# Kernel tuning notes

Measured on AMD Instinct MI355X. Metric: run time of the kernel, lower is better.

The kernel has to match this reference:

```python
import jax, jax.numpy as jnp
import numpy as np

B, Q, V, H, U = 4, 256, 2048, 512, 128

def setup_inputs() -> dict:
    key = jax.random.key(0)
    ks = jax.random.split(key, 5)
    return {
        "queries": jax.random.normal(ks[0], (B, Q, H), dtype=jnp.float32),
        "values": jax.random.normal(ks[1], (B, V, H), dtype=jnp.float32),
        "w1": jax.random.normal(ks[2], (H, U), dtype=jnp.float32) / np.sqrt(H),
        "w2": jax.random.normal(ks[3], (H, U), dtype=jnp.float32) / np.sqrt(H),
        "v": jax.random.normal(ks[4], (U,), dtype=jnp.float32) / np.sqrt(U),
    }

def reference(queries, values, w1, w2, v):
    # Project queries and values first (cheap GEMMs), then broadcast-add.
    pq = jnp.einsum("bqh,hu->bqu", queries, w1)          # [B,Q,U]
    pv = jnp.einsum("bvh,hu->bvu", values, w2)           # [B,V,U]
    # added_qv: [B,Q,V,U] -- the large intermediate the original materializes
    scores = jnp.einsum("bqvu,u->bqv", jnp.tanh(pq[:, :, None, :] + pv[:, None, :, :]), v)
    attn = jax.nn.softmax(scores, axis=-1)               # softmax over V (last axis, as tf.nn.softmax)
    return jnp.einsum("bqv,bvh->bqh", attn, values)      # [B,Q,H]
```

## Files before the change

### kernel.cpp

```cpp
#include <hip/hip_runtime.h>

#define BB 4
#define QQ 256
#define VV 2048
#define HH 512
#define UU 128

#define C2E   2.8853900817779268f
#define LOG2E 1.4426950408889634f

__device__ __forceinline__ void fma4(float4& a, float s, const float4& w) {
    a.x = fmaf(s, w.x, a.x);
    a.y = fmaf(s, w.y, a.y);
    a.z = fmaf(s, w.z, a.z);
    a.w = fmaf(s, w.w, a.w);
}
__device__ __forceinline__ void fma2s(float2& a, float s, const float2& w) {
    a.x = fmaf(s, w.x, a.x);
    a.y = fmaf(s, w.y, a.y);
}
__device__ __forceinline__ float2 rcp2(float2 x) {
    return make_float2(__builtin_amdgcn_rcpf(x.x), __builtin_amdgcn_rcpf(x.y));
}
__device__ __forceinline__ float2 mul2(float2 a, float2 b) { return make_float2(a.x*b.x, a.y*b.y); }
__device__ __forceinline__ float2 muls(float2 a, float s)  { return make_float2(a.x*s, a.y*s); }
__device__ __forceinline__ float2 fma2(float2 a, float2 b, float2 c) {
    return make_float2(fmaf(a.x, b.x, c.x), fmaf(a.y, b.y, c.y));
}
__device__ __forceinline__ float2 fmas(float2 a, float s, float2 c) {
    return make_float2(fmaf(a.x, s, c.x), fmaf(a.y, s, c.y));
}

__global__ __launch_bounds__(128) void proj_kernel(const float* __restrict__ queries,
                                                   const float* __restrict__ values,
                                                   const float* __restrict__ w1,
                                                   const float* __restrict__ w2,
                                                   float* __restrict__ pqI,
                                                   float* __restrict__ pvI,
                                                   float* __restrict__ denom) {
    __shared__ float smem[32 * 20 + 32 * 128];
    float (*As)[20] = (float(*)[20])smem;
    float* Ws = smem + 32 * 20;
    float (*Ls)[20] = (float(*)[20])smem;

    const int bid = blockIdx.x;
    const int tid = threadIdx.x;
    if (bid == 0) {
        *(float4*)&denom[tid * 8]     = make_float4(0.f, 0.f, 0.f, 0.f);
        *(float4*)&denom[tid * 8 + 4] = make_float4(0.f, 0.f, 0.f, 0.f);
    }

    const bool isv = (bid < 512);
    const float* A; const float* W; int b, r0, ROWS; float* Ob;
    if (isv) {
        b = bid >> 7; r0 = (bid & 127) * 16;
        A = values + ((size_t)(b * VV + r0)) * HH;  W = w2;
        Ob = pvI + (size_t)b * UU * VV;  ROWS = VV;
    } else {
        const int q = bid - 512;
        b = q >> 4; r0 = (q & 15) * 16;
        A = queries + ((size_t)(b * QQ + r0)) * HH; W = w1;
        Ob = pqI + (size_t)b * UU * QQ;  ROWS = QQ;
    }

    const int tx = tid & 31;
    const int ty = tid >> 5;
    float4 acc[4];
#pragma unroll
    for (int j = 0; j < 4; j++) acc[j] = make_float4(0.f, 0.f, 0.f, 0.f);

    for (int k0 = 0; k0 < HH; k0 += 32) {
        {
            const int r = tid >> 3, kk4 = (tid & 7) * 4;
            const float4 a = *(const float4*)&A[(size_t)r * HH + k0 + kk4];
            As[kk4 + 0][r] = a.x; As[kk4 + 1][r] = a.y;
            As[kk4 + 2][r] = a.z; As[kk4 + 3][r] = a.w;
        }
#pragma unroll
        for (int t = 0; t < 8; t++) {
            const int f = tid + t * 128;
            const int kk = f >> 5, u4 = (f & 31) * 4;
            *(float4*)&Ws[kk * 128 + u4] = *(const float4*)&W[(size_t)(k0 + kk) * UU + u4];
        }
        __syncthreads();
#pragma unroll
        for (int kk = 0; kk < 32; kk++) {
            const float4 a = *(const float4*)&As[kk][ty * 4];
            const float4 w = *(const float4*)&Ws[kk * 128 + tx * 4];
            fma4(acc[0], a.x, w);
            fma4(acc[1], a.y, w);
            fma4(acc[2], a.z, w);
            fma4(acc[3], a.w, w);
        }
        __syncthreads();
    }
#pragma unroll
    for (int j = 0; j < 4; j++) {
        const float aa[4] = {acc[j].x, acc[j].y, acc[j].z, acc[j].w};
#pragma unroll
        for (int i = 0; i < 4; i++)
            Ls[tx * 4 + i][ty * 4 + j] = __builtin_amdgcn_exp2f(aa[i] * C2E);
    }
    __syncthreads();
#pragma unroll
    for (int t = 0; t < 4; t++) {
        const int idx = tid + t * 128;
        const int g = idx >> 4, r = idx & 15;
        float4 o;
        o.x = Ls[4 * g + 0][r]; o.y = Ls[4 * g + 1][r];
        o.z = Ls[4 * g + 2][r]; o.w = Ls[4 * g + 3][r];
        *(float4*)&Ob[((size_t)g * ROWS + r0 + r) * 4] = o;
    }
}

__global__ __launch_bounds__(256, 4) void fused_kernel(const float* __restrict__ pqI,
                                                       const float* __restrict__ pvI,
                                                       const float* __restrict__ vvec,
                                                       const float* __restrict__ values,
                                                       float* __restrict__ slab,
                                                       float* __restrict__ denom) {
    __shared__ float att[128][16];
    __shared__ float wred[2][16];
    const int tid = threadIdx.x;
    const int bid = blockIdx.x;
    const int vs = bid & 15, qb = (bid >> 4) & 15, b = bid >> 8;
    const int qbase = qb * 16, vbase = vs * 128;

    const int vloc = tid & 127, uh = tid >> 7;
    const int v = vbase + vloc;

    float vsum = 0.0f;
#pragma unroll
    for (int u4 = 0; u4 < UU; u4 += 4) {
        const float4 t = *(const float4*)&vvec[u4];
        vsum += t.x + t.y + t.z + t.w;
    }

    const float* pv4 = pvI + (size_t)b * UU * VV + (size_t)v * 4;
    const float* pq4 = pqI + (size_t)b * UU * QQ + (size_t)qbase * 4;

    float2 acc[8];
#pragma unroll
    for (int p = 0; p < 8; p++) acc[p] = make_float2(0.f, 0.f);

    const int G0 = uh * 16;
    float4 ev = *(const float4*)&pv4[(size_t)G0 * VV * 4];

    for (int g = 0; g < 16; g++) {
        const int G = G0 + g;
        const float* eqp = &pq4[(size_t)G * QQ * 4];
        float4 evn;
        if (g < 15) evn = *(const float4*)&pv4[(size_t)(G + 1) * VV * 4];
        const float4 wq = *(const float4*)&vvec[G * 4];
        const float w0 = 2.f * wq.x, w1 = 2.f * wq.y;
        const float w2 = 2.f * wq.z, w3 = 2.f * wq.w;
#pragma unroll
        for (int p = 0; p < 8; p++) {
            const float4 e0 = *(const float4*)&eqp[(2 * p) * 4];
            const float4 e1 = *(const float4*)&eqp[(2 * p + 1) * 4];
            const float2 a1 = make_float2(fmaf(e0.x, ev.x, 1.f), fmaf(e1.x, ev.x, 1.f));
            const float2 b1 = make_float2(fmaf(e0.y, ev.y, 1.f), fmaf(e1.y, ev.y, 1.f));
            const float2 c1 = make_float2(fmaf(e0.z, ev.z, 1.f), fmaf(e1.z, ev.z, 1.f));
            const float2 d1 = make_float2(fmaf(e0.w, ev.w, 1.f), fmaf(e1.w, ev.w, 1.f));
            const float2 pab = mul2(a1, b1), pcd = mul2(c1, d1);
            const float2 nab = fmas(a1, w1, muls(b1, w0));
            const float2 ncd = fmas(c1, w3, muls(d1, w2));
            const float2 num = fma2(nab, pcd, mul2(ncd, pab));
            const float2 den = mul2(pab, pcd);
            acc[p] = fma2(num, rcp2(den), acc[p]);
        }
        ev = evn;
    }

    if (uh == 1) {
#pragma unroll
        for (int p = 0; p < 8; p++)
            *(float2*)&att[vloc][2 * p] = acc[p];
    }
    __syncthreads();
    if (uh == 0) {
#pragma unroll
        for (int p = 0; p < 8; p++) {
            const float2 hi = *(const float2*)&att[vloc][2 * p];
            float2 e;
            e.x = __builtin_amdgcn_exp2f((vsum - (acc[p].x + hi.x)) * LOG2E);
            e.y = __builtin_amdgcn_exp2f((vsum - (acc[p].y + hi.y)) * LOG2E);
            *(float2*)&att[vloc][2 * p] = e;
            acc[p] = e;
        }
#pragma unroll
        for (int off = 1; off < 64; off <<= 1) {
#pragma unroll
            for (int p = 0; p < 8; p++) {
                acc[p].x += __shfl_xor(acc[p].x, off, 64);
                acc[p].y += __shfl_xor(acc[p].y, off, 64);
            }
        }
        if ((tid & 63) == 0) {
            const int w = tid >> 6;
#pragma unroll
            for (int p = 0; p < 8; p++) {
                wred[w][2 * p + 0] = acc[p].x;
                wred[w][2 * p + 1] = acc[p].y;
            }
        }
    }
    __syncthreads();
    if (tid < 16)
        atomicAdd(&denom[b * QQ + qbase + tid], wred[0][tid] + wred[1][tid]);

    const int h0 = tid * 2;
    const float* vp = values + ((size_t)(b * VV + vbase)) * HH + h0;

    float2 oacc[16];
#pragma unroll
    for (int j = 0; j < 16; j++) oacc[j] = make_float2(0.f, 0.f);

#pragma unroll 2
    for (int vv = 0; vv < 128; vv++) {
        const float2 w = *(const float2*)&vp[(size_t)vv * HH];
        const float4 a0 = *(const float4*)&att[vv][0];
        const float4 a1 = *(const float4*)&att[vv][4];
        const float4 a2 = *(const float4*)&att[vv][8];
        const float4 a3 = *(const float4*)&att[vv][12];
        fma2s(oacc[0],  a0.x, w); fma2s(oacc[1],  a0.y, w);
        fma2s(oacc[2],  a0.z, w); fma2s(oacc[3],  a0.w, w);
        fma2s(oacc[4],  a1.x, w); fma2s(oacc[5],  a1.y, w);
        fma2s(oacc[6],  a1.z, w); fma2s(oacc[7],  a1.w, w);
        fma2s(oacc[8],  a2.x, w); fma2s(oacc[9],  a2.y, w);
        fma2s(oacc[10], a2.z, w); fma2s(oacc[11], a2.w, w);
        fma2s(oacc[12], a3.x, w); fma2s(oacc[13], a3.y, w);
        fma2s(oacc[14], a3.z, w); fma2s(oacc[15], a3.w, w);
    }

    float* sp = slab + (size_t)vs * (BB * QQ * HH);
#pragma unroll
    for (int j = 0; j < 16; j++) {
        *(float2*)&sp[((size_t)(b * QQ + qbase + j)) * HH + h0] = oacc[j];
    }
}

__global__ __launch_bounds__(256) void reduce_kernel(const float* __restrict__ slab,
                                                     const float* __restrict__ denom,
                                                     float* __restrict__ out) {
    const int i = blockIdx.x * 256 + threadIdx.x;
    const float r = __builtin_amdgcn_rcpf(denom[i >> 7]);
    const float4* s4 = (const float4*)slab;
    float4 s = s4[i];
#pragma unroll
    for (int k = 1; k < 16; k++) {
        const float4 p = s4[(size_t)k * (BB * QQ * HH / 4) + i];
        s.x += p.x; s.y += p.y; s.z += p.z; s.w += p.w;
    }
    s.x *= r; s.y *= r; s.z *= r; s.w *= r;
    ((float4*)out)[i] = s;
}

extern "C" void kernel_launch(void* const* d_in, const int* in_sizes, int n_in,
                              void* d_out, int out_size, void* d_ws, size_t ws_size,
                              hipStream_t stream) {
    const float* queries = (const float*)d_in[0];
    const float* values  = (const float*)d_in[1];
    const float* w1      = (const float*)d_in[2];
    const float* w2      = (const float*)d_in[3];
    const float* vvec    = (const float*)d_in[4];
    float* out = (float*)d_out;

    float* ws    = (float*)d_ws;
    float* pqI   = ws;
    float* pvI   = pqI + BB * UU * QQ;
    float* denom = pvI + (size_t)BB * UU * VV;
    float* slab  = denom + BB * QQ;

    proj_kernel<<<512 + 64, 128, 0, stream>>>(queries, values, w1, w2, pqI, pvI, denom);
    fused_kernel<<<BB * (QQ / 16) * (VV / 128), 256, 0, stream>>>(pqI, pvI, vvec, values,
                                                                  slab, denom);
    reduce_kernel<<<(BB * QQ * HH) / 4 / 256, 256, 0, stream>>>(slab, denom, out);
}
```

Before: 177.4 us.

## Use split-bf16 MFMA for attention-times-values with pre-transposed values

The attention-weighted sum over values moves from scalar FP32 FMAs to bf16 MFMA 16x16x32 instructions. FP32 accuracy is approximated with a hi/lo split using three MFMAs per step. The projection kernel gains extra blocks that transpose values into hi and lo bf16 arrays laid out as [B,H,V]. Attention weights are stored as hi/lo bf16 in shared memory in the same layout. This cuts ALU work in the dominant loop, but adds a transpose pass, extra workspace traffic, and small precision loss from dropping the lo*lo term.

```diff
diff --git a/kernel.cpp b/kernel.cpp
--- a/kernel.cpp
+++ b/kernel.cpp
@@ -9,16 +9,15 @@
 #define C2E   2.8853900817779268f
 #define LOG2E 1.4426950408889634f
 
+typedef __attribute__((ext_vector_type(8))) short bf16x8;
+typedef __attribute__((ext_vector_type(4))) float f32x4;
+
 __device__ __forceinline__ void fma4(float4& a, float s, const float4& w) {
     a.x = fmaf(s, w.x, a.x);
     a.y = fmaf(s, w.y, a.y);
     a.z = fmaf(s, w.z, a.z);
     a.w = fmaf(s, w.w, a.w);
 }
-__device__ __forceinline__ void fma2s(float2& a, float s, const float2& w) {
-    a.x = fmaf(s, w.x, a.x);
-    a.y = fmaf(s, w.y, a.y);
-}
 __device__ __forceinline__ float2 rcp2(float2 x) {
     return make_float2(__builtin_amdgcn_rcpf(x.x), __builtin_amdgcn_rcpf(x.y));
 }
@@ -29,6 +28,14 @@
 }
 __device__ __forceinline__ float2 fmas(float2 a, float s, float2 c) {
     return make_float2(fmaf(a.x, s, c.x), fmaf(a.y, s, c.y));
+}
+__device__ __forceinline__ unsigned short f2bf(float x) {
+    unsigned int u = __float_as_uint(x);
+    u += 0x7fff + ((u >> 16) & 1);
+    return (unsigned short)(u >> 16);
+}
+__device__ __forceinline__ float bf2f(unsigned short h) {
+    return __uint_as_float(((unsigned int)h) << 16);
 }
 
 __global__ __launch_bounds__(128) void proj_kernel(const float* __restrict__ queries,
@@ -37,14 +44,44 @@
                                                    const float* __restrict__ w2,
                                                    float* __restrict__ pqI,
                                                    float* __restrict__ pvI,
+                                                   unsigned short* __restrict__ vThi,
+                                                   unsigned short* __restrict__ vTlo,
                                                    float* __restrict__ denom) {
-    __shared__ float smem[32 * 20 + 32 * 128];
+    __shared__ float smem[4736];
+    const int bid = blockIdx.x;
+    const int tid = threadIdx.x;
+
+    if (bid >= 576) {
+        const int t = bid - 576;
+        const int b = t >> 8, tt = t & 255;
+        const int v0 = (tt >> 3) * 64, h0 = (tt & 7) * 64;
+        float (*S)[68] = (float(*)[68])smem;
+#pragma unroll
+        for (int j = 0; j < 8; j++) {
+            const int f = tid + j * 128;
+            const int vr = f >> 4, c4 = (f & 15) * 4;
+            const float4 a = *(const float4*)&values[((size_t)(b * VV + v0 + vr)) * HH + h0 + c4];
+            S[vr][c4 + 0] = a.x; S[vr][c4 + 1] = a.y;
+            S[vr][c4 + 2] = a.z; S[vr][c4 + 3] = a.w;
+        }
+        __syncthreads();
+        const int hr = tid >> 1, half = (tid & 1) * 32;
+        const size_t rowo = ((size_t)(b * HH + h0 + hr)) * VV + v0 + half;
+#pragma unroll
+        for (int c = 0; c < 32; c += 2) {
+            const float x0 = S[half + c][hr], x1 = S[half + c + 1][hr];
+            const unsigned short h0b = f2bf(x0), h1b = f2bf(x1);
+            const unsigned short l0b = f2bf(x0 - bf2f(h0b)), l1b = f2bf(x1 - bf2f(h1b));
+            *(ushort2*)&vThi[rowo + c] = make_ushort2(h0b, h1b);
+            *(ushort2*)&vTlo[rowo + c] = make_ushort2(l0b, l1b);
+        }
+        return;
+    }
+
     float (*As)[20] = (float(*)[20])smem;
     float* Ws = smem + 32 * 20;
     float (*Ls)[20] = (float(*)[20])smem;
 
-    const int bid = blockIdx.x;
-    const int tid = threadIdx.x;
     if (bid == 0) {
         *(float4*)&denom[tid * 8]     = make_float4(0.f, 0.f, 0.f, 0.f);
         *(float4*)&denom[tid * 8 + 4] = make_float4(0.f, 0.f, 0.f, 0.f);
@@ -116,10 +153,13 @@
 __global__ __launch_bounds__(256, 4) void fused_kernel(const float* __restrict__ pqI,
                                                        const float* __restrict__ pvI,
                                                        const float* __restrict__ vvec,
-                                                       const float* __restrict__ values,
+                                                       const unsigned short* __restrict__ vThi,
+                                                       const unsigned short* __restrict__ vTlo,
                                                        float* __restrict__ slab,
                                                        float* __restrict__ denom) {
-    __shared__ float att[128][16];
+    __shared__ float cbuf[128][16];
+    __shared__ __align__(16) unsigned short attHi[16][136];
+    __shared__ __align__(16) unsigned short attLo[16][136];
     __shared__ float wred[2][16];
     const int tid = threadIdx.x;
     const int bid = blockIdx.x;
@@ -175,17 +215,21 @@
     if (uh == 1) {
 #pragma unroll
         for (int p = 0; p < 8; p++)
-            *(float2*)&att[vloc][2 * p] = acc[p];
+            *(float2*)&cbuf[vloc][2 * p] = acc[p];
     }
     __syncthreads();
     if (uh == 0) {
 #pragma unroll
         for (int p = 0; p < 8; p++) {
-            const float2 hi = *(const float2*)&att[vloc][2 * p];
+            const float2 hi = *(const float2*)&cbuf[vloc][2 * p];
             float2 e;
             e.x = __builtin_amdgcn_exp2f((vsum - (acc[p].x + hi.x)) * LOG2E);
             e.y = __builtin_amdgcn_exp2f((vsum - (acc[p].y + hi.y)) * LOG2E);
-            *(float2*)&att[vloc][2 * p] = e;
+            const unsigned short hx = f2bf(e.x), hy = f2bf(e.y);
+            attHi[2 * p + 0][vloc] = hx;
+            attHi[2 * p + 1][vloc] = hy;
+            attLo[2 * p + 0][vloc] = f2bf(e.x - bf2f(hx));
+            attLo[2 * p + 1][vloc] = f2bf(e.y - bf2f(hy));
             acc[p] = e;
         }
 #pragma unroll
@@ -209,34 +253,42 @@
     if (tid < 16)
         atomicAdd(&denom[b * QQ + qbase + tid], wred[0][tid] + wred[1][tid]);
 
-    const int h0 = tid * 2;
-    const float* vp = values + ((size_t)(b * VV + vbase)) * HH + h0;
-
-    float2 oacc[16];
-#pragma unroll
-    for (int j = 0; j < 16; j++) oacc[j] = make_float2(0.f, 0.f);
-
-#pragma unroll 2
-    for (int vv = 0; vv < 128; vv++) {
-        const float2 w = *(const float2*)&vp[(size_t)vv * HH];
-        const float4 a0 = *(const float4*)&att[vv][0];
-        const float4 a1 = *(const float4*)&att[vv][4];
-        const float4 a2 = *(const float4*)&att[vv][8];
-        const float4 a3 = *(const float4*)&att[vv][12];
-        fma2s(oacc[0],  a0.x, w); fma2s(oacc[1],  a0.y, w);
-        fma2s(oacc[2],  a0.z, w); fma2s(oacc[3],  a0.w, w);
-        fma2s(oacc[4],  a1.x, w); fma2s(oacc[5],  a1.y, w);
-        fma2s(oacc[6],  a1.z, w); fma2s(oacc[7],  a1.w, w);
-        fma2s(oacc[8],  a2.x, w); fma2s(oacc[9],  a2.y, w);
-        fma2s(oacc[10], a2.z, w); fma2s(oacc[11], a2.w, w);
-        fma2s(oacc[12], a3.x, w); fma2s(oacc[13], a3.y, w);
-        fma2s(oacc[14], a3.z, w); fma2s(oacc[15], a3.w, w);
-    }
-
-    float* sp = slab + (size_t)vs * (BB * QQ * HH);
-#pragma unroll
-    for (int j = 0; j < 16; j++) {
-        *(float2*)&sp[((size_t)(b * QQ + qbase + j)) * HH + h0] = oacc[j];
+    const int lane = tid & 63, wv = tid >> 6;
+    const int m = lane & 15, quad = lane >> 4;
+
+    bf16x8 ahi[4], alo[4];
+#pragma unroll
+    for (int s = 0; s < 4; s++) {
+        const int k0 = s * 32 + quad * 8;
+        ahi[s] = *(const bf16x8*)(const void*)&attHi[m][k0];
+        alo[s] = *(const bf16x8*)(const void*)&attLo[m][k0];
+    }
+
+    const unsigned short* vhb = vThi + ((size_t)b * HH + wv * 128) * VV + vbase;
+    const unsigned short* vlb = vTlo + ((size_t)b * HH + wv * 128) * VV + vbase;
+    float* sp = slab + (size_t)vs * (BB * QQ * HH) + ((size_t)(b * QQ + qbase)) * HH;
+
+#pragma unroll
+    for (int t8 = 0; t8 < 8; t8++) {
+        const int hrel = t8 * 16 + m;
+        const unsigned short* ph = vhb + (size_t)hrel * VV;
+        const unsigned short* pl = vlb + (size_t)hrel * VV;
+        f32x4 c = {0.f, 0.f, 0.f, 0.f};
+#pragma unroll
+        for (int s = 0; s < 4; s++) {
+            const int kb = s * 32 + quad * 8;
+            const bf16x8 bh = *(const bf16x8*)(const void*)&ph[kb];
+            const bf16x8 bl = *(const bf16x8*)(const void*)&pl[kb];
+            c = __builtin_amdgcn_mfma_f32_16x16x32_bf16(alo[s], bh, c, 0, 0, 0);
+            c = __builtin_amdgcn_mfma_f32_16x16x32_bf16(ahi[s], bl, c, 0, 0, 0);
+            c = __builtin_amdgcn_mfma_f32_16x16x32_bf16(ahi[s], bh, c, 0, 0, 0);
+        }
+        const int hh = wv * 128 + hrel;
+#pragma unroll
+        for (int r = 0; r < 4; r++) {
+            const int q = quad * 4 + r;
+            sp[(size_t)q * HH + hh] = c[r];
+        }
     }
 }
 
@@ -271,9 +323,12 @@
     float* pvI   = pqI + BB * UU * QQ;
     float* denom = pvI + (size_t)BB * UU * VV;
     float* slab  = denom + BB * QQ;
-
-    proj_kernel<<<512 + 64, 128, 0, stream>>>(queries, values, w1, w2, pqI, pvI, denom);
-    fused_kernel<<<BB * (QQ / 16) * (VV / 128), 256, 0, stream>>>(pqI, pvI, vvec, values,
-                                                                  slab, denom);
+    unsigned short* vThi = (unsigned short*)(slab + (size_t)16 * BB * QQ * HH);
+    unsigned short* vTlo = vThi + (size_t)BB * HH * VV;
+
+    proj_kernel<<<576 + 1024, 128, 0, stream>>>(queries, values, w1, w2, pqI, pvI,
+                                                vThi, vTlo, denom);
+    fused_kernel<<<BB * (QQ / 16) * (VV / 128), 256, 0, stream>>>(pqI, pvI, vvec,
+                                                                  vThi, vTlo, slab, denom);
     reduce_kernel<<<(BB * QQ * HH) / 4 / 256, 256, 0, stream>>>(slab, denom, out);
 }
```

Result: no change. 178.3 us (+0.5%).
